# Optimization experiments

Hardware: AMD Instinct MI355X
Metric: run time of the kernel (lower is better)

The kernel has to match this reference:

```python
import jax, jax.numpy as jnp
import numpy as np

DIM = 1024
HEADS = 16
DK = DIM // HEADS

def _layernorm(x, g, b, eps=1e-5):
    mu = jnp.mean(x, axis=-1, keepdims=True)
    var = jnp.mean((x - mu) ** 2, axis=-1, keepdims=True)
    return (x - mu) * jax.lax.rsqrt(var + eps) * g + b

def _split_heads(x):
    b, n, _ = x.shape
    return x.reshape(b, n, HEADS, DK).transpose(0, 2, 1, 3)  # b h n d

def setup_inputs() -> dict:
    key = jax.random.key(0)
    ks = jax.random.split(key, 16)
    s = 0.02
    inp = {
        'text_tensor': jax.random.normal(ks[0], (8, 512, DIM), jnp.float32),
        'vision_tensor': jax.random.normal(ks[1], (8, 1024, DIM), jnp.float32),
        'norm1_g': jnp.ones((DIM,), jnp.float32),
        'norm1_b': jnp.zeros((DIM,), jnp.float32),
        'norm2_g': jnp.ones((DIM,), jnp.float32),
        'norm2_b': jnp.zeros((DIM,), jnp.float32),
    }
    names = ['q1', 'k1', 'v1', 'q2', 'k2', 'v2']
    for i, nm in enumerate(names):
        inp[f'W_{nm}'] = jax.random.normal(ks[2 + i], (DIM, DIM), jnp.float32) * s
        inp[f'b_{nm}'] = jnp.zeros((DIM,), jnp.float32)
    return inp

def reference(text_tensor, vision_tensor, norm1_g, norm1_b, norm2_g, norm2_b,
              W_q1, b_q1, W_k1, b_k1, W_v1, b_v1,
              W_q2, b_q2, W_k2, b_k2, W_v2, b_v2):
    text_residual = text_tensor
    vision_residual = vision_tensor
    t = _layernorm(text_tensor, norm1_g, norm1_b)
    v = _layernorm(vision_tensor, norm2_g, norm2_b)
    # projections (torch Linear: x @ W.T + b)
    tq = _split_heads(t @ W_q1.T + b_q1)
    tk = _split_heads(t @ W_k1.T + b_k1)
    tv = _split_heads(t @ W_v1.T + b_v1)
    vq = _split_heads(v @ W_q2.T + b_q2)
    vk = _split_heads(v @ W_k2.T + b_k2)
    vv = _split_heads(v @ W_v2.T + b_v2)
    scale = DK ** -0.5
    # text queries attend to vision keys/values
    s1 = jnp.einsum('bhnd,bhmd->bhnm', tq, vk) * scale
    a1 = jnp.einsum('bhnm,bhmd->bhnd', jax.nn.softmax(s1, axis=-1), vv)
    # vision queries attend to text keys/values
    s2 = jnp.einsum('bhmd,bhnd->bhmn', vq, tk) * scale
    a2 = jnp.einsum('bhmn,bhnd->bhmd', jax.nn.softmax(s2, axis=-1), tv)
    b_, h_, n_, d_ = a1.shape
    attention_1 = a1.transpose(0, 2, 1, 3).reshape(b_, n_, h_ * d_)
    m_ = a2.shape[2]
    attention_2 = a2.transpose(0, 2, 1, 3).reshape(b_, m_, h_ * d_)
    return attention_1, attention_2, text_residual, vision_residual
```

## Files before the change

### kernel.cpp

```cpp
#include <hip/hip_runtime.h>
#include <stdint.h>


#define DIM 1024
#define HEADS 16
#define DK 64
#define BATCH 8
#define NTXT 512
#define NVIS 1024

typedef __attribute__((ext_vector_type(8))) short bf16x8;
typedef __attribute__((ext_vector_type(4))) float f32x4;
typedef __attribute__((ext_vector_type(4))) unsigned short u16x4;
typedef __attribute__((ext_vector_type(4))) unsigned int u32x4;

__device__ inline unsigned short f2bf(float f) {
    unsigned u = __builtin_bit_cast(unsigned, f);
    u += 0x7fffu + ((u >> 16) & 1u);
    return (unsigned short)(u >> 16);
}
__device__ inline f32x4 mfma16(bf16x8 a, bf16x8 b, f32x4 c) {
    return __builtin_amdgcn_mfma_f32_16x16x32_bf16(a, b, c, 0, 0, 0);
}
__device__ inline void gl_lds16(const unsigned short* gp, unsigned short* lp) {
    const auto* g1 = reinterpret_cast<const __attribute__((address_space(1))) unsigned int*>(
        reinterpret_cast<uintptr_t>(gp));
    auto* l3 = reinterpret_cast<__attribute__((address_space(3))) unsigned int*>(
        reinterpret_cast<uintptr_t>(lp));
    __builtin_amdgcn_global_load_lds(g1, l3, 16, 0, 0);
}

struct WPtrs { const float* w[6]; };

__global__ __launch_bounds__(256) void prep_kernel(
        WPtrs p, unsigned short* __restrict__ Wc,
        const float* __restrict__ text, const float* __restrict__ n1g,
        const float* __restrict__ n1b, unsigned short* __restrict__ tno,
        float* __restrict__ tres,
        const float* __restrict__ vision, const float* __restrict__ n2g,
        const float* __restrict__ n2b, unsigned short* __restrict__ vno,
        float* __restrict__ vres) {
    int gid = blockIdx.x;
    int tid = threadIdx.x;
    if (gid < 6144) {
        int g = gid >> 10;
        int i = (gid & 1023) * 256 + tid;
        float4 v = ((const float4*)p.w[g])[i];
        u16x4 o;
        o[0] = f2bf(v.x); o[1] = f2bf(v.y); o[2] = f2bf(v.z); o[3] = f2bf(v.w);
        *(u16x4*)(Wc + (size_t)g * (DIM * DIM) + (size_t)i * 4) = o;
        return;
    }
    const float* x; const float* g; const float* bta;
    unsigned short* xn; float* res; int row;
    if (gid < 10240) { row = gid - 6144;  x = text;   g = n1g; bta = n1b; xn = tno; res = tres; }
    else             { row = gid - 10240; x = vision; g = n2g; bta = n2b; xn = vno; res = vres; }
    const float4* xr = (const float4*)(x + (size_t)row * DIM);
    float4 v = xr[tid];
    float s = v.x + v.y + v.z + v.w;
    float ss = v.x * v.x + v.y * v.y + v.z * v.z + v.w * v.w;
#pragma unroll
    for (int m = 1; m < 64; m <<= 1) { s += __shfl_xor(s, m); ss += __shfl_xor(ss, m); }
    __shared__ float red[8];
    int wave = tid >> 6, lane = tid & 63;
    if (lane == 0) { red[wave] = s; red[4 + wave] = ss; }
    __syncthreads();
    s = red[0] + red[1] + red[2] + red[3];
    ss = red[4] + red[5] + red[6] + red[7];
    float mu = s * (1.0f / DIM);
    float var = ss * (1.0f / DIM) - mu * mu;
    float rinv = rsqrtf(var + 1e-5f);
    float4 gv = ((const float4*)g)[tid];
    float4 bv = ((const float4*)bta)[tid];
    ((float4*)(res + (size_t)row * DIM))[tid] = v;
    u16x4 o;
    o[0] = f2bf((v.x - mu) * rinv * gv.x + bv.x);
    o[1] = f2bf((v.y - mu) * rinv * gv.y + bv.y);
    o[2] = f2bf((v.z - mu) * rinv * gv.z + bv.z);
    o[3] = f2bf((v.w - mu) * rinv * gv.w + bv.w);
    *(u16x4*)(xn + (size_t)row * DIM + tid * 4) = o;
}

struct GemmParams {
    const unsigned short* A[2];
    const unsigned short* W;
    const float* bias[6];
    unsigned short* out[6];
};

__global__ __launch_bounds__(256, 3) void gemm_qkv_kernel(GemmParams P) {
    int bid = blockIdx.x;
    int xcd = bid & 7;
    int idx = bid >> 3;
    int g, tm, tn;
    if (idx < 96) {
        int col = idx >> 2, mi = idx & 3;
        g = col >> 3; tn = col & 7; tm = xcd * 4 + mi;
    } else {
        int j = idx - 96;
        int col = j >> 3, mi = j & 7;
        g = 3 + (col >> 3); tn = col & 7; tm = xcd * 8 + mi;
    }
    const unsigned short* A = P.A[g < 3 ? 0 : 1];
    const unsigned short* Ap = A + (size_t)tm * 128 * DIM;
    const unsigned short* Wp = P.W + (size_t)g * (DIM * DIM) + (size_t)tn * 128 * DIM;

    __shared__ __align__(16) unsigned short As[128][64];
    __shared__ __align__(16) unsigned short Bs[128][64];

    int tid = threadIdx.x;
    int wave = tid >> 6, lane = tid & 63;
    int wm = (wave & 1) * 64, wn = (wave >> 1) * 64;
    int col16 = lane & 15, quad = lane >> 4;

    int sbase = wave * 64 + lane;
    size_t ga[4];
    unsigned short* lA[4];
    unsigned short* lB[4];
#pragma unroll
    for (int i = 0; i < 4; i++) {
        int s = sbase + i * 256;
        int row = s >> 3;
        int c = (s & 7) ^ (row & 7);
        ga[i] = (size_t)row * DIM + (size_t)c * 8;
        lA[i] = &As[0][0] + (size_t)s * 8;
        lB[i] = &Bs[0][0] + (size_t)s * 8;
    }

    f32x4 zero = {0.f, 0.f, 0.f, 0.f};
    f32x4 acc[4][4];
#pragma unroll
    for (int i = 0; i < 4; i++)
#pragma unroll
        for (int j = 0; j < 4; j++) acc[i][j] = zero;

    for (int k0 = 0; k0 < DIM; k0 += 64) {
        __syncthreads();
#pragma unroll
        for (int i = 0; i < 4; i++) {
            gl_lds16(Ap + ga[i] + k0, lA[i]);
            gl_lds16(Wp + ga[i] + k0, lB[i]);
        }
        __syncthreads();
#pragma unroll
        for (int ks = 0; ks < 2; ks++) {
            bf16x8 af[4], bfr[4];
#pragma unroll
            for (int mi = 0; mi < 4; mi++) {
                int r = wm + mi * 16 + col16;
                int p = (ks * 4 + quad) ^ (r & 7);
                af[mi] = *(const bf16x8*)&As[r][p * 8];
            }
#pragma unroll
            for (int ni = 0; ni < 4; ni++) {
                int r = wn + ni * 16 + col16;
                int p = (ks * 4 + quad) ^ (r & 7);
                bfr[ni] = *(const bf16x8*)&Bs[r][p * 8];
            }
#pragma unroll
            for (int mi = 0; mi < 4; mi++)
#pragma unroll
                for (int ni = 0; ni < 4; ni++)
                    acc[mi][ni] = mfma16(af[mi], bfr[ni], acc[mi][ni]);
        }
    }

    const float* bias = P.bias[g];
    unsigned short* out = P.out[g];
    float qs = (g == 0 || g == 3) ? 0.18033688f : 1.0f;
    float bv[4];
#pragma unroll
    for (int ni = 0; ni < 4; ni++) bv[ni] = bias[tn * 128 + wn + ni * 16 + col16];

    if (g == 2 || g == 5) {
        int N = (g == 2) ? NTXT : NVIS;
#pragma unroll
        for (int mi = 0; mi < 4; mi++) {
            int row0 = tm * 128 + wm + mi * 16 + quad * 4;
            int b = row0 / N;
            int npos = row0 - b * N;
#pragma unroll
            for (int ni = 0; ni < 4; ni++) {
                int col = tn * 128 + wn + ni * 16 + col16;
                int h = col >> 6, d = col & 63;
                u16x4 pk;
#pragma unroll
                for (int reg = 0; reg < 4; reg++) pk[reg] = f2bf(acc[mi][ni][reg] + bv[ni]);
                *(u16x4*)(out + ((size_t)((b * HEADS + h) * DK + d)) * N + npos) = pk;
            }
        }
    } else {
#pragma unroll
        for (int mi = 0; mi < 4; mi++) {
#pragma unroll
            for (int reg = 0; reg < 4; reg++) {
                int row = tm * 128 + wm + mi * 16 + quad * 4 + reg;
#pragma unroll
                for (int ni = 0; ni < 4; ni++) {
                    out[(size_t)row * DIM + tn * 128 + wn + ni * 16 + col16] =
                        f2bf((acc[mi][ni][reg] + bv[ni]) * qs);
                }
            }
        }
    }
}

__global__ __launch_bounds__(256, 4) void attn_kernel(
        const unsigned short* __restrict__ Q1, const unsigned short* __restrict__ K1,
        const unsigned short* __restrict__ V1t, float* __restrict__ O1,
        const unsigned short* __restrict__ Q2, const unsigned short* __restrict__ K2,
        const unsigned short* __restrict__ V2t, float* __restrict__ O2) {
    int bid = blockIdx.x;
    const unsigned short* Q; const unsigned short* K; const unsigned short* Vt;
    float* Out; int Nq, Nkv;
    if (bid < 512) { Q = Q1; K = K1; Vt = V1t; Out = O1; Nq = NTXT; Nkv = NVIS; }
    else { bid -= 512; Q = Q2; K = K2; Vt = V2t; Out = O2; Nq = NVIS; Nkv = NTXT; }
    int bh = bid & 127;
    int qt = bid >> 7;
    int b = bh >> 4, h = bh & 15;
    int tid = threadIdx.x;
    int wave = tid >> 6, lane = tid & 63;
    int col16 = lane & 15, quad = lane >> 4;

    __shared__ __align__(16) unsigned short KV[2][2][8][512];

    const unsigned short* qbase =
        Q + ((size_t)(b * Nq + qt * 128 + wave * 32 + col16)) * DIM + h * DK;
    bf16x8 qa[2][2];
#pragma unroll
    for (int mg = 0; mg < 2; mg++) {
        qa[mg][0] = *(const bf16x8*)(qbase + (size_t)mg * 16 * DIM + quad * 8);
        qa[mg][1] = *(const bf16x8*)(qbase + (size_t)mg * 16 * DIM + 32 + quad * 8);
    }

    int r0 = ((col16 >> 2) << 3) + (col16 & 3);

    int whh = wave >> 1, wpr = wave & 1;
    const unsigned short* Ksrc =
        K + ((size_t)b * Nkv + 32 * whh + 4 * wpr + r0) * DIM + h * DK + quad * 8;
    const unsigned short* Vsrc =
        Vt + (size_t)(b * HEADS + h) * DK * Nkv
           + (size_t)(2 * wpr * 16 + col16) * Nkv + 32 * whh + quad * 8;
    unsigned short* ldsK0 = &KV[0][0][2 * wave][0];
    unsigned short* ldsK1 = &KV[0][0][2 * wave + 1][0];
    unsigned short* ldsV0 = &KV[0][1][2 * wave][0];
    unsigned short* ldsV1 = &KV[0][1][2 * wave + 1][0];
    const int PSTRIDE = 2 * 8 * 512;

    f32x4 zero = {0.f, 0.f, 0.f, 0.f};
    f32x4 o[2][4];
#pragma unroll
    for (int mg = 0; mg < 2; mg++)
#pragma unroll
        for (int d = 0; d < 4; d++) o[mg][d] = zero;
    float lsum[2] = {0.f, 0.f};

    auto STAGE = [&](int p, int nb) {
        const unsigned short* ks = Ksrc + (size_t)nb * DIM;
        const unsigned short* vs = Vsrc + nb;
        int po = p * PSTRIDE;
        gl_lds16(ks,            ldsK0 + po);
        gl_lds16(ks + 32,       ldsK1 + po);
        gl_lds16(vs,            ldsV0 + po);
        gl_lds16(vs + 16 * Nkv, ldsV1 + po);
    };

    auto COMPUTE = [&](int p) {
        const unsigned short* base = &KV[p][0][0][0] + lane * 8;
#pragma unroll
        for (int hh = 0; hh < 2; hh++) {
            bf16x8 ka0 = *(const bf16x8*)(base + (hh * 4 + 0) * 512);
            bf16x8 ka1 = *(const bf16x8*)(base + (hh * 4 + 1) * 512);
            bf16x8 kb0 = *(const bf16x8*)(base + (hh * 4 + 2) * 512);
            bf16x8 kb1 = *(const bf16x8*)(base + (hh * 4 + 3) * 512);
            bf16x8 vf[4];
#pragma unroll
            for (int d = 0; d < 4; d++)
                vf[d] = *(const bf16x8*)(base + 4096 + (hh * 4 + d) * 512);
#pragma unroll
            for (int mg = 0; mg < 2; mg++) {
                f32x4 ca = zero, cb = zero;
                ca = mfma16(ka0, qa[mg][0], ca);
                ca = mfma16(ka1, qa[mg][1], ca);
                cb = mfma16(kb0, qa[mg][0], cb);
                cb = mfma16(kb1, qa[mg][1], cb);
                float p0 = __builtin_amdgcn_exp2f(ca[0]);
                float p1 = __builtin_amdgcn_exp2f(ca[1]);
                float p2 = __builtin_amdgcn_exp2f(ca[2]);
                float p3 = __builtin_amdgcn_exp2f(ca[3]);
                float p4 = __builtin_amdgcn_exp2f(cb[0]);
                float p5 = __builtin_amdgcn_exp2f(cb[1]);
                float p6 = __builtin_amdgcn_exp2f(cb[2]);
                float p7 = __builtin_amdgcn_exp2f(cb[3]);
                lsum[mg] += ((p0 + p1) + (p2 + p3)) + ((p4 + p5) + (p6 + p7));
                unsigned int w0, w1, w2, w3;
                asm("v_cvt_pk_bf16_f32 %0, %1, %2" : "=v"(w0) : "v"(p0), "v"(p1));
                asm("v_cvt_pk_bf16_f32 %0, %1, %2" : "=v"(w1) : "v"(p2), "v"(p3));
                asm("v_cvt_pk_bf16_f32 %0, %1, %2" : "=v"(w2) : "v"(p4), "v"(p5));
                asm("v_cvt_pk_bf16_f32 %0, %1, %2" : "=v"(w3) : "v"(p6), "v"(p7));
                u32x4 pw = {w0, w1, w2, w3};
                bf16x8 pf = __builtin_bit_cast(bf16x8, pw);
#pragma unroll
                for (int d = 0; d < 4; d++) o[mg][d] = mfma16(pf, vf[d], o[mg][d]);
            }
        }
    };

    int NT = Nkv >> 6;
    STAGE(0, 0);
    __syncthreads();
    int par = 0;
    for (int t = 0; t + 1 < NT; t++) {
        STAGE(par ^ 1, (t + 1) << 6);
        COMPUTE(par);
        __syncthreads();
        par ^= 1;
    }
    COMPUTE(par);

#pragma unroll
    for (int mg = 0; mg < 2; mg++) {
        float l = lsum[mg];
        l += __shfl_xor(l, 16);
        l += __shfl_xor(l, 32);
#pragma unroll
        for (int reg = 0; reg < 4; reg++) {
            float inv = 1.0f / __shfl(l, quad * 4 + reg);
            int nrow = qt * 128 + wave * 32 + mg * 16 + quad * 4 + reg;
            float* op = Out + ((size_t)(b * Nq + nrow)) * DIM + h * DK;
#pragma unroll
            for (int d = 0; d < 4; d++) op[d * 16 + col16] = o[mg][d][reg] * inv;
        }
    }
}

extern "C" void kernel_launch(void* const* d_in, const int* in_sizes, int n_in,
                              void* d_out, int out_size, void* d_ws, size_t ws_size,
                              hipStream_t stream) {
    const float* text   = (const float*)d_in[0];
    const float* vision = (const float*)d_in[1];
    const float* n1g = (const float*)d_in[2];
    const float* n1b = (const float*)d_in[3];
    const float* n2g = (const float*)d_in[4];
    const float* n2b = (const float*)d_in[5];
    const float* W[6];
    const float* bias[6];
    for (int i = 0; i < 6; i++) {
        W[i]    = (const float*)d_in[6 + 2 * i];
        bias[i] = (const float*)d_in[7 + 2 * i];
    }

    float* out = (float*)d_out;
    float* a1   = out;
    float* a2   = out + 4194304;
    float* tres = out + 12582912;
    float* vres = out + 16777216;

    char* ws = (char*)d_ws;
    unsigned short* Wc  = (unsigned short*)(ws);
    unsigned short* tno = (unsigned short*)(ws + 12582912);
    unsigned short* vno = (unsigned short*)(ws + 20971520);
    unsigned short* tq  = (unsigned short*)(ws + 37748736);
    unsigned short* tk  = (unsigned short*)(ws + 46137344);
    unsigned short* tvT = (unsigned short*)(ws + 54525952);
    unsigned short* vq  = (unsigned short*)(ws + 62914560);
    unsigned short* vk  = (unsigned short*)(ws + 79691776);
    unsigned short* vvT = (unsigned short*)(ws + 96468992);

    WPtrs wp;
    for (int i = 0; i < 6; i++) wp.w[i] = W[i];
    prep_kernel<<<18432, 256, 0, stream>>>(wp, Wc,
                                           text, n1g, n1b, tno, tres,
                                           vision, n2g, n2b, vno, vres);

    GemmParams gp;
    gp.A[0] = tno; gp.A[1] = vno; gp.W = Wc;
    for (int i = 0; i < 6; i++) gp.bias[i] = bias[i];
    gp.out[0] = tq; gp.out[1] = tk; gp.out[2] = tvT;
    gp.out[3] = vq; gp.out[4] = vk; gp.out[5] = vvT;
    gemm_qkv_kernel<<<2304, 256, 0, stream>>>(gp);

    attn_kernel<<<1536, 256, 0, stream>>>(tq, vk, vvT, a1, vq, tk, tvT, a2);
}
```

Baseline: 311.4 us.

## Stage K/V tiles through registers with two-ahead prefetch instead of direct global-to-LDS loads

The attention kernel stops using direct global-to-LDS copies for K and V tiles. It now loads each tile into registers two iterations ahead and writes it to the alternate LDS buffer one iteration ahead, so global load latency is hidden behind a full compute step. This adds register pressure, since four 16-byte vectors stay live, and replaces the async LDS path with explicit ds_write instructions that the waves must issue themselves.

Measured after the change: 310.9 us. Within noise of the previous version (-0.1%).

```diff
diff --git a/kernel.cpp b/kernel.cpp
--- a/kernel.cpp
+++ b/kernel.cpp
@@ -241,10 +241,10 @@
     const unsigned short* Vsrc =
         Vt + (size_t)(b * HEADS + h) * DK * Nkv
            + (size_t)(2 * wpr * 16 + col16) * Nkv + 32 * whh + quad * 8;
-    unsigned short* ldsK0 = &KV[0][0][2 * wave][0];
-    unsigned short* ldsK1 = &KV[0][0][2 * wave + 1][0];
-    unsigned short* ldsV0 = &KV[0][1][2 * wave][0];
-    unsigned short* ldsV1 = &KV[0][1][2 * wave + 1][0];
+    unsigned short* ldsK0 = &KV[0][0][2 * wave][0] + (size_t)lane * 8;
+    unsigned short* ldsK1 = &KV[0][0][2 * wave + 1][0] + (size_t)lane * 8;
+    unsigned short* ldsV0 = &KV[0][1][2 * wave][0] + (size_t)lane * 8;
+    unsigned short* ldsV1 = &KV[0][1][2 * wave + 1][0] + (size_t)lane * 8;
     const int PSTRIDE = 2 * 8 * 512;
 
     f32x4 zero = {0.f, 0.f, 0.f, 0.f};
@@ -255,14 +255,22 @@
         for (int d = 0; d < 4; d++) o[mg][d] = zero;
     float lsum[2] = {0.f, 0.f};
 
-    auto STAGE = [&](int p, int nb) {
-        const unsigned short* ks = Ksrc + (size_t)nb * DIM;
-        const unsigned short* vs = Vsrc + nb;
+    bf16x8 rk0, rk1, rv0, rv1;
+
+    auto LOADR = [&](int t) {
+        const unsigned short* ks = Ksrc + (((size_t)t) << 6) * DIM;
+        const unsigned short* vs = Vsrc + (t << 6);
+        rk0 = *(const bf16x8*)(ks);
+        rk1 = *(const bf16x8*)(ks + 32);
+        rv0 = *(const bf16x8*)(vs);
+        rv1 = *(const bf16x8*)(vs + 16 * Nkv);
+    };
+    auto WRITE = [&](int p) {
         int po = p * PSTRIDE;
-        gl_lds16(ks,            ldsK0 + po);
-        gl_lds16(ks + 32,       ldsK1 + po);
-        gl_lds16(vs,            ldsV0 + po);
-        gl_lds16(vs + 16 * Nkv, ldsV1 + po);
+        *(bf16x8*)(ldsK0 + po) = rk0;
+        *(bf16x8*)(ldsK1 + po) = rk1;
+        *(bf16x8*)(ldsV0 + po) = rv0;
+        *(bf16x8*)(ldsV1 + po) = rv1;
     };
 
     auto COMPUTE = [&](int p) {
@@ -307,16 +315,20 @@
     };
 
     int NT = Nkv >> 6;
-    STAGE(0, 0);
+    LOADR(0);
+    WRITE(0);
+    LOADR(1);
     __syncthreads();
     int par = 0;
-    for (int t = 0; t + 1 < NT; t++) {
-        STAGE(par ^ 1, (t + 1) << 6);
+    for (int t = 0; t < NT; t++) {
+        if (t + 1 < NT) {
+            WRITE(par ^ 1);
+            if (t + 2 < NT) LOADR(t + 2);
+        }
         COMPUTE(par);
-        __syncthreads();
+        if (t + 1 < NT) __syncthreads();
         par ^= 1;
     }
-    COMPUTE(par);
 
 #pragma unroll
     for (int mg = 0; mg < 2; mg++) {
```
